# Kernel optimization log

Hardware: AMD Instinct MI355X
Metric: run time of the kernel (lower is better)

The kernel has to match this reference:

```python
import jax, jax.numpy as jnp
import numpy as np

B = 64            # decoding sequences (1 query token each)
H = 32            # query heads
HKV = 8           # kv heads (GQA)
D = 128           # head dim
BS = 16           # block size (tokens per cache block)
BPB = 64          # blocks per sequence
L = BS * BPB      # max kv length = 1024
NBLK = B * BPB    # total cache blocks = 4096
SCALE = 0.08838834764831845  # 1/sqrt(128)


def setup_inputs() -> dict:
    key = jax.random.key(0)
    k1, k2, k3, k4, k5, k6 = jax.random.split(key, 6)
    q = jax.random.normal(k1, (B, H * D), dtype=jnp.float32)
    k = jax.random.normal(k2, (B, HKV * D), dtype=jnp.float32)
    v = jax.random.normal(k3, (B, HKV * D), dtype=jnp.float32)
    k_cache = jax.random.normal(k4, (NBLK, BS, HKV, D), dtype=jnp.float32)
    v_cache = jax.random.normal(k5, (NBLK, BS, HKV, D), dtype=jnp.float32)
    # each sequence owns a disjoint run of blocks
    block_tables = jnp.arange(B * BPB, dtype=jnp.int64).reshape(B, BPB)
    # context length includes the newly stored token; at least 1
    context_lens = jax.random.randint(k6, (B,), 1, L + 1).astype(jnp.int64)
    # slot of the newest token at position context_len-1
    pos = context_lens - 1
    slot_mapping = block_tables[jnp.arange(B), pos // BS] * BS + pos % BS
    return {"q": q, "k": k, "v": v, "k_cache": k_cache, "v_cache": v_cache,
            "block_tables": block_tables, "context_lens": context_lens,
            "slot_mapping": slot_mapping}


def reference(q, k, v, k_cache, v_cache, block_tables, context_lens, slot_mapping):
    G = H // HKV
    # store new k/v into the paged cache (store_kvcache_pytorch)
    kc = k_cache.reshape(-1, HKV, D).at[slot_mapping].set(k.reshape(-1, HKV, D))
    vc = v_cache.reshape(-1, HKV, D).at[slot_mapping].set(v.reshape(-1, HKV, D))
    # block-table gather: slot(t) = block_table[t//BS]*BS + t%BS
    t = jnp.arange(L)
    slots = block_tables[:, t // BS] * BS + (t % BS)          # [B, L]
    ks = kc[slots]                                            # [B, L, HKV, D]
    vs = vc[slots]                                            # [B, L, HKV, D]
    # GQA attention: q head h uses kv head h // G
    qr = q.reshape(B, HKV, G, D)
    scores = jnp.einsum('bhgd,blhd->bhgl', qr, ks) * SCALE    # [B, HKV, G, L]
    mask = t[None, :] < context_lens[:, None]                 # [B, L]
    scores = jnp.where(mask[:, None, None, :], scores, jnp.float32(-1e30))
    p = jax.nn.softmax(scores, axis=-1)
    o = jnp.einsum('bhgl,blhd->bhgd', p, vs)                  # [B, HKV, G, D]
    return o.reshape(B, H * D)
```

## Files before the change

kernel.cpp:

```cpp
#include <hip/hip_runtime.h>

#define BB    64
#define HH    32
#define HKVH  8
#define GG    4
#define DD    128
#define BSZ   16
#define BPB   64
#define LMAX  1024
#define SCALEF 0.08838834764831845f

__device__ __forceinline__ long long ld_i(const void* p, long long i, bool is64) {
  return is64 ? ((const long long*)p)[i] : (long long)((const int*)p)[i];
}

__global__ __launch_bounds__(256)
void attn_partial(const float* __restrict__ q,
                  const float* __restrict__ knew,
                  const float* __restrict__ vnew,
                  const float* __restrict__ kcache,
                  const float* __restrict__ vcache,
                  const void*  __restrict__ bt,
                  const void*  __restrict__ ctxl,
                  float* __restrict__ o_part,
                  float* __restrict__ ml_part,
                  int NP, int PART)
{
  const int part = blockIdx.x;
  const int kvh  = blockIdx.y;
  const int b    = blockIdx.z;
  const int tid  = threadIdx.x;
  const int lane = tid & 63;
  const int wave = tid >> 6;
  const int gi   = lane >> 4;
  const int j    = lane & 15;
  const int group = wave * 4 + gi;

  const bool is64 = (((const int*)bt)[1] == 0);
  const int ctx = (int)ld_i(ctxl, b, is64);

  const float* qb = q + ((size_t)b * HH + (size_t)kvh * GG) * DD + j * 8;
  float4 q0[GG], q1[GG];
#pragma unroll
  for (int g = 0; g < GG; ++g) {
    q0[g] = *(const float4*)(qb + g * DD);
    q1[g] = *(const float4*)(qb + g * DD + 4);
  }

  float m[GG], lsum[GG];
  float4 o0[GG], o1[GG];
#pragma unroll
  for (int g = 0; g < GG; ++g) {
    m[g] = -1e30f; lsum[g] = 0.f;
    o0[g] = make_float4(0.f, 0.f, 0.f, 0.f);
    o1[g] = make_float4(0.f, 0.f, 0.f, 0.f);
  }

  const int pbase = part * PART;
  int nt = ctx - pbase;
  if (nt > PART) nt = PART;
  const int iters = (nt > 0) ? ((nt + 15) >> 4) : 0;
  const int ctxm1 = ctx - 1;
  const float* newrow_k = knew + ((size_t)b * HKVH + kvh) * DD;
  const float* newrow_v = vnew + ((size_t)b * HKVH + kvh) * DD;

  for (int it = 0; it < iters; ++it) {
    const int t = pbase + it * 16 + group;
    if (t < ctx) {
      const float* krow;
      const float* vrow;
      if (t == ctxm1) {
        krow = newrow_k; vrow = newrow_v;
      } else {
        const long long blk = ld_i(bt, (long long)b * BPB + (t >> 4), is64);
        const size_t off = (((size_t)blk * BSZ + (t & 15)) * HKVH + kvh) * DD;
        krow = kcache + off;
        vrow = vcache + off;
      }
      const float4 ka = *(const float4*)(krow + j * 8);
      const float4 kb = *(const float4*)(krow + j * 8 + 4);
      const float4 va = *(const float4*)(vrow + j * 8);
      const float4 vb = *(const float4*)(vrow + j * 8 + 4);

      float s[GG];
#pragma unroll
      for (int g = 0; g < GG; ++g) {
        s[g] = q0[g].x * ka.x + q0[g].y * ka.y + q0[g].z * ka.z + q0[g].w * ka.w
             + q1[g].x * kb.x + q1[g].y * kb.y + q1[g].z * kb.z + q1[g].w * kb.w;
      }
#pragma unroll
      for (int off = 8; off >= 1; off >>= 1) {
#pragma unroll
        for (int g = 0; g < GG; ++g) s[g] += __shfl_xor(s[g], off, 16);
      }
#pragma unroll
      for (int g = 0; g < GG; ++g) {
        const float sg = s[g] * SCALEF;
        const float mo = m[g];
        const float mn = fmaxf(mo, sg);
        const float p  = __expf(sg - mn);
        if (mn > mo) {
          const float al = __expf(mo - mn);
          lsum[g] *= al;
          o0[g].x *= al; o0[g].y *= al; o0[g].z *= al; o0[g].w *= al;
          o1[g].x *= al; o1[g].y *= al; o1[g].z *= al; o1[g].w *= al;
        }
        m[g] = mn;
        lsum[g] += p;
        o0[g].x += p * va.x; o0[g].y += p * va.y; o0[g].z += p * va.z; o0[g].w += p * va.w;
        o1[g].x += p * vb.x; o1[g].y += p * vb.y; o1[g].z += p * vb.z; o1[g].w += p * vb.w;
      }
    }
  }

  __shared__ float sm_o[16][GG][DD];
  __shared__ float sm_m[16][GG];
  __shared__ float sm_l[16][GG];
#pragma unroll
  for (int g = 0; g < GG; ++g) {
    *(float4*)&sm_o[group][g][j * 8]     = o0[g];
    *(float4*)&sm_o[group][g][j * 8 + 4] = o1[g];
  }
  if (j == 0) {
#pragma unroll
    for (int g = 0; g < GG; ++g) { sm_m[group][g] = m[g]; sm_l[group][g] = lsum[g]; }
  }
  __syncthreads();

#pragma unroll
  for (int rep = 0; rep < 2; ++rep) {
    const int idx = tid + rep * 256;
    const int g = idx >> 7;
    const int d = idx & 127;
    float M = -1e30f;
#pragma unroll
    for (int s2 = 0; s2 < 16; ++s2) M = fmaxf(M, sm_m[s2][g]);
    float Ls = 0.f, Os = 0.f;
#pragma unroll
    for (int s2 = 0; s2 < 16; ++s2) {
      const float w = __expf(sm_m[s2][g] - M);
      Ls += sm_l[s2][g] * w;
      Os += sm_o[s2][g][d] * w;
    }
    const size_t pidx = (((size_t)b * HKVH + kvh) * NP + part) * GG + g;
    o_part[pidx * DD + d] = Os;
    if (d == 0) { ml_part[pidx * 2] = M; ml_part[pidx * 2 + 1] = Ls; }
  }
}

__global__ __launch_bounds__(256)
void attn_combine(const float* __restrict__ o_part,
                  const float* __restrict__ ml_part,
                  float* __restrict__ out, int NP)
{
  const int blk = blockIdx.x;
  const int tid = threadIdx.x;
#pragma unroll
  for (int rep = 0; rep < 2; ++rep) {
    const int idx = tid + rep * 256;
    const int g = idx >> 7;
    const int d = idx & 127;
    const size_t base = (size_t)blk * NP;
    float M = -1e30f;
    for (int p = 0; p < NP; ++p)
      M = fmaxf(M, ml_part[((base + p) * GG + g) * 2]);
    float Ls = 0.f, Os = 0.f;
    for (int p = 0; p < NP; ++p) {
      const size_t pidx = (base + p) * GG + g;
      const float w = __expf(ml_part[pidx * 2] - M);
      Ls += ml_part[pidx * 2 + 1] * w;
      Os += o_part[pidx * DD + d] * w;
    }
    out[(size_t)blk * GG * DD + g * DD + d] = Os / Ls;
  }
}

extern "C" void kernel_launch(void* const* d_in, const int* in_sizes, int n_in,
                              void* d_out, int out_size, void* d_ws, size_t ws_size,
                              hipStream_t stream)
{
  const float* q  = (const float*)d_in[0];
  const float* kn = (const float*)d_in[1];
  const float* vn = (const float*)d_in[2];
  const float* kc = (const float*)d_in[3];
  const float* vc = (const float*)d_in[4];
  const void*  bt = d_in[5];
  const void*  cl = d_in[6];
  float* out = (float*)d_out;

  int NP = 8;
  while (NP > 1) {
    size_t need = (size_t)BB * HKVH * NP * GG * (DD + 2) * sizeof(float);
    if (need <= ws_size) break;
    NP >>= 1;
  }
  const int PART = LMAX / NP;

  float* o_part  = (float*)d_ws;
  float* ml_part = o_part + (size_t)BB * HKVH * NP * GG * DD;

  dim3 grid1(NP, HKVH, BB);
  attn_partial<<<grid1, 256, 0, stream>>>(q, kn, vn, kc, vc, bt, cl,
                                          o_part, ml_part, NP, PART);
  attn_combine<<<BB * HKVH, 256, 0, stream>>>(o_part, ml_part, out, NP);
}
```

Measured before the change: 497.0 us.

## Software-pipeline K/V row loads and switch softmax to exp2 domain

Restructures the partial attention loop to prefetch the next iteration's K/V rows and the block-table entry two iterations ahead, so global-load latency overlaps with the dot products and online softmax. Invalid tokens are masked with a large negative score instead of being branched around, and out-of-range positions point at the new-token row. Scores are pre-scaled by log2(e) so exp2f is used throughout, including in both combine stages. The cost is extra registers for the double-buffered float4s, which may reduce occupancy.

Result: no change. 500.2 us (+0.6%).

```diff
diff --git a/kernel.cpp b/kernel.cpp
--- a/kernel.cpp
+++ b/kernel.cpp
@@ -9,6 +9,8 @@
 #define BPB   64
 #define LMAX  1024
 #define SCALEF 0.08838834764831845f
+#define LOG2E  1.4426950408889634f
+#define SCALE2 (SCALEF * LOG2E)
 
 __device__ __forceinline__ long long ld_i(const void* p, long long i, bool is64) {
   return is64 ? ((const long long*)p)[i] : (long long)((const int*)p)[i];
@@ -38,6 +40,7 @@
 
   const bool is64 = (((const int*)bt)[1] == 0);
   const int ctx = (int)ld_i(ctxl, b, is64);
+  const int ctxm1 = ctx - 1;
 
   const float* qb = q + ((size_t)b * HH + (size_t)kvh * GG) * DD + j * 8;
   float4 q0[GG], q1[GG];
@@ -60,57 +63,76 @@
   int nt = ctx - pbase;
   if (nt > PART) nt = PART;
   const int iters = (nt > 0) ? ((nt + 15) >> 4) : 0;
-  const int ctxm1 = ctx - 1;
-  const float* newrow_k = knew + ((size_t)b * HKVH + kvh) * DD;
-  const float* newrow_v = vnew + ((size_t)b * HKVH + kvh) * DD;
+
+  const float* nk = knew + ((size_t)b * HKVH + kvh) * DD + j * 8;
+  const float* nv = vnew + ((size_t)b * HKVH + kvh) * DD + j * 8;
+  const long long btbase = (long long)b * BPB + (pbase >> 4);
+  const int lo = j * 8;
+
+  auto kptr = [&](int it, long long blkv) -> const float* {
+    const int t = pbase + it * 16 + group;
+    if (t >= ctxm1) return nk;
+    return kcache + (((size_t)blkv * BSZ + group) * HKVH + kvh) * DD + lo;
+  };
+  auto vptr = [&](int it, long long blkv) -> const float* {
+    const int t = pbase + it * 16 + group;
+    if (t >= ctxm1) return nv;
+    return vcache + (((size_t)blkv * BSZ + group) * HKVH + kvh) * DD + lo;
+  };
+
+  float4 kA, kB, vA, vB, kA2, kB2, vA2, vB2;
+  long long blk_c = (iters > 0) ? ld_i(bt, btbase, is64) : 0;
+  long long blk_n = (iters > 1) ? ld_i(bt, btbase + 1, is64) : 0;
+  if (iters > 0) {
+    const float* kr = kptr(0, blk_c);
+    const float* vr = vptr(0, blk_c);
+    kA = *(const float4*)kr; kB = *(const float4*)(kr + 4);
+    vA = *(const float4*)vr; vB = *(const float4*)(vr + 4);
+  }
 
   for (int it = 0; it < iters; ++it) {
+    if (it + 1 < iters) {
+      const float* kr = kptr(it + 1, blk_n);
+      const float* vr = vptr(it + 1, blk_n);
+      kA2 = *(const float4*)kr; kB2 = *(const float4*)(kr + 4);
+      vA2 = *(const float4*)vr; vB2 = *(const float4*)(vr + 4);
+    }
+    const long long blk_2 = (it + 2 < iters) ? ld_i(bt, btbase + it + 2, is64) : 0;
+
     const int t = pbase + it * 16 + group;
-    if (t < ctx) {
-      const float* krow;
-      const float* vrow;
-      if (t == ctxm1) {
-        krow = newrow_k; vrow = newrow_v;
-      } else {
-        const long long blk = ld_i(bt, (long long)b * BPB + (t >> 4), is64);
-        const size_t off = (((size_t)blk * BSZ + (t & 15)) * HKVH + kvh) * DD;
-        krow = kcache + off;
-        vrow = vcache + off;
+    const bool valid = (t <= ctxm1);
+
+    float s[GG];
+#pragma unroll
+    for (int g = 0; g < GG; ++g) {
+      s[g] = q0[g].x * kA.x + q0[g].y * kA.y + q0[g].z * kA.z + q0[g].w * kA.w
+           + q1[g].x * kB.x + q1[g].y * kB.y + q1[g].z * kB.z + q1[g].w * kB.w;
+    }
+#pragma unroll
+    for (int off = 8; off >= 1; off >>= 1) {
+#pragma unroll
+      for (int g = 0; g < GG; ++g) s[g] += __shfl_xor(s[g], off, 16);
+    }
+#pragma unroll
+    for (int g = 0; g < GG; ++g) {
+      const float sg = valid ? s[g] * SCALE2 : -3.0e38f;
+      const float mo = m[g];
+      const float mn = fmaxf(mo, sg);
+      const float p  = exp2f(sg - mn);
+      if (mn > mo) {
+        const float al = exp2f(mo - mn);
+        lsum[g] *= al;
+        o0[g].x *= al; o0[g].y *= al; o0[g].z *= al; o0[g].w *= al;
+        o1[g].x *= al; o1[g].y *= al; o1[g].z *= al; o1[g].w *= al;
       }
-      const float4 ka = *(const float4*)(krow + j * 8);
-      const float4 kb = *(const float4*)(krow + j * 8 + 4);
-      const float4 va = *(const float4*)(vrow + j * 8);
-      const float4 vb = *(const float4*)(vrow + j * 8 + 4);
-
-      float s[GG];
-#pragma unroll
-      for (int g = 0; g < GG; ++g) {
-        s[g] = q0[g].x * ka.x + q0[g].y * ka.y + q0[g].z * ka.z + q0[g].w * ka.w
-             + q1[g].x * kb.x + q1[g].y * kb.y + q1[g].z * kb.z + q1[g].w * kb.w;
-      }
-#pragma unroll
-      for (int off = 8; off >= 1; off >>= 1) {
-#pragma unroll
-        for (int g = 0; g < GG; ++g) s[g] += __shfl_xor(s[g], off, 16);
-      }
-#pragma unroll
-      for (int g = 0; g < GG; ++g) {
-        const float sg = s[g] * SCALEF;
-        const float mo = m[g];
-        const float mn = fmaxf(mo, sg);
-        const float p  = __expf(sg - mn);
-        if (mn > mo) {
-          const float al = __expf(mo - mn);
-          lsum[g] *= al;
-          o0[g].x *= al; o0[g].y *= al; o0[g].z *= al; o0[g].w *= al;
-          o1[g].x *= al; o1[g].y *= al; o1[g].z *= al; o1[g].w *= al;
-        }
-        m[g] = mn;
-        lsum[g] += p;
-        o0[g].x += p * va.x; o0[g].y += p * va.y; o0[g].z += p * va.z; o0[g].w += p * va.w;
-        o1[g].x += p * vb.x; o1[g].y += p * vb.y; o1[g].z += p * vb.z; o1[g].w += p * vb.w;
-      }
-    }
+      m[g] = mn;
+      lsum[g] += p;
+      o0[g].x += p * vA.x; o0[g].y += p * vA.y; o0[g].z += p * vA.z; o0[g].w += p * vA.w;
+      o1[g].x += p * vB.x; o1[g].y += p * vB.y; o1[g].z += p * vB.z; o1[g].w += p * vB.w;
+    }
+
+    kA = kA2; kB = kB2; vA = vA2; vB = vB2;
+    blk_c = blk_n; blk_n = blk_2;
   }
 
   __shared__ float sm_o[16][GG][DD];
@@ -118,8 +140,8 @@
   __shared__ float sm_l[16][GG];
 #pragma unroll
   for (int g = 0; g < GG; ++g) {
-    *(float4*)&sm_o[group][g][j * 8]     = o0[g];
-    *(float4*)&sm_o[group][g][j * 8 + 4] = o1[g];
+    *(float4*)&sm_o[group][g][lo]     = o0[g];
+    *(float4*)&sm_o[group][g][lo + 4] = o1[g];
   }
   if (j == 0) {
 #pragma unroll
@@ -138,7 +160,7 @@
     float Ls = 0.f, Os = 0.f;
 #pragma unroll
     for (int s2 = 0; s2 < 16; ++s2) {
-      const float w = __expf(sm_m[s2][g] - M);
+      const float w = exp2f(sm_m[s2][g] - M);
       Ls += sm_l[s2][g] * w;
       Os += sm_o[s2][g][d] * w;
     }
@@ -167,7 +189,7 @@
     float Ls = 0.f, Os = 0.f;
     for (int p = 0; p < NP; ++p) {
       const size_t pidx = (base + p) * GG + g;
-      const float w = __expf(ml_part[pidx * 2] - M);
+      const float w = exp2f(ml_part[pidx * 2] - M);
       Ls += ml_part[pidx * 2 + 1] * w;
       Os += o_part[pidx * DD + d] * w;
     }
```
